# Optimization experiments

Measured on AMD Instinct MI355X. Metric: run time of the kernel, lower is better.

## Reference

```python
import jax, jax.numpy as jnp
import numpy as np

N_NODES = 100000
MAX_DEG = 128
BATCH = 16384
NUM_SAMPLES = 25


def setup_inputs() -> dict:
    key = jax.random.key(0)
    k1, k2, k3 = jax.random.split(key, 3)
    adj_weight = jax.random.uniform(k1, (N_NODES, MAX_DEG), dtype=jnp.float32)
    adj_info = jax.random.randint(k2, (N_NODES, MAX_DEG), 0, N_NODES, dtype=jnp.int32)
    ids = jax.random.randint(k3, (BATCH,), 0, N_NODES, dtype=jnp.int64)
    return {
        "adj_weight": adj_weight,
        "adj_info": adj_info,
        "ids": ids,
        "num_samples": NUM_SAMPLES,
    }


def reference(adj_weight, adj_info, ids, num_samples):
    # Gather per-node neighbor lists and weights: [B, max_deg]
    adj_lists = adj_info[ids]
    adj_weight_lists = adj_weight[ids]
    # tf.multinomial(tf.log(w), num_samples): categorical sampling with
    # replacement, probabilities proportional to weights.
    logits = jnp.log(adj_weight_lists)  # [B, max_deg]
    skey = jax.random.key(42)
    # categorical over last axis; draw num_samples per row -> [B, num_samples]
    idx = jax.random.categorical(
        skey, logits, axis=-1, shape=(num_samples, ids.shape[0])
    ).T
    # Gather sampled neighbor ids (equivalent to the flattened bias+gather trick)
    res = jnp.take_along_axis(adj_lists, idx, axis=1)  # [B, num_samples]
    return res
```

## Files before the change

kernel.cpp:

```cpp
#include <hip/hip_runtime.h>
#include <stdint.h>


#define MAXDEG 128

__device__ __forceinline__ uint32_t rotl32(uint32_t x, int r) {
  return __builtin_rotateleft32(x, r);
}

__device__ __forceinline__ uint32_t tf_bits(uint32_t i) {
  uint32_t x0, x1;
  x1 = i + 42u;
  x0 = x1;
  x1 = rotl32(x1, 13) ^ x0;
  x0 += x1; x1 = rotl32(x1, 15) ^ x0;
  x0 += x1; x1 = rotl32(x1, 26) ^ x0;
  x0 += x1; x1 = rotl32(x1,  6) ^ x0;
  x1 += 0x1BD11BF1u; x0 = x0 + x1 + 42u;
  x1 = rotl32(x1, 17) ^ x0;
  x0 += x1; x1 = rotl32(x1, 29) ^ x0;
  x0 += x1; x1 = rotl32(x1, 16) ^ x0;
  x0 += x1; x1 = rotl32(x1, 24) ^ x0;
  x1 += 2u; x0 = x0 + x1 + 0x1BD11BF0u;
  x1 = rotl32(x1, 13) ^ x0;
  x0 += x1; x1 = rotl32(x1, 15) ^ x0;
  x0 += x1; x1 = rotl32(x1, 26) ^ x0;
  x0 += x1; x1 = rotl32(x1,  6) ^ x0;
  x1 += 45u; x0 = x0 + x1;
  x1 = rotl32(x1, 17) ^ x0;
  x0 += x1; x1 = rotl32(x1, 29) ^ x0;
  x0 += x1; x1 = rotl32(x1, 16) ^ x0;
  x0 += x1; x1 = rotl32(x1, 24) ^ x0;
  x1 += 0x1BD11BF4u; x0 = x0 + x1 + 42u;
  x1 = rotl32(x1, 13) ^ x0;
  x0 += x1; x1 = rotl32(x1, 15) ^ x0;
  x0 += x1; x1 = rotl32(x1, 26) ^ x0;
  x0 += x1; x1 = rotl32(x1,  6) ^ x0;
  return (x0 + 0x1BD11BF0u) ^ (x1 + 5u);
}

__device__ __forceinline__ float uniform_from_bits(uint32_t bits) {
  uint32_t fb = (bits >> 9) | 0x3f800000u;
  float f = __uint_as_float(fb) - 1.0f;
  return fmaxf(f, 1.17549435e-38f);
}

__device__ __forceinline__ float zscore(float lwp, uint32_t bits) {
  const float l = __log2f(uniform_from_bits(bits));
  const float t = __log2f(-l);
  return __builtin_fmaf(-0.69314718056f, t, lwp);
}

template <int CTRL>
__device__ __forceinline__ float dpp_max_step(float z) {
  const int t = __builtin_amdgcn_update_dpp(0, __float_as_int(z), CTRL, 0xF, 0xF, true);
  return fmaxf(z, __int_as_float(t));
}

__device__ __forceinline__ float swz_max16(float z) {
  return fmaxf(z, __int_as_float(
      __builtin_amdgcn_ds_swizzle(__float_as_int(z), 0x401F)));
}

__device__ __attribute__((noinline)) void resolve_f64(
    float4 wv, uint32_t sbase, int l, int lane, int storeLane,
    const int* __restrict__ adj_info, long long nid,
    int* __restrict__ out, long long outIdx) {
  const uint32_t bits0 = tf_bits(sbase + 0u);
  const uint32_t bits1 = tf_bits(sbase + 1u);
  const uint32_t bits2 = tf_bits(sbase + 2u);
  const uint32_t bits3 = tf_bits(sbase + 3u);
  double bz = log((double)wv.x) - log(-log((double)uniform_from_bits(bits0)));
  int bd = 4 * l;
  const double Z1 = log((double)wv.y) - log(-log((double)uniform_from_bits(bits1)));
  if (Z1 > bz) { bz = Z1; bd = 4 * l + 1; }
  const double Z2 = log((double)wv.z) - log(-log((double)uniform_from_bits(bits2)));
  if (Z2 > bz) { bz = Z2; bd = 4 * l + 2; }
  const double Z3 = log((double)wv.w) - log(-log((double)uniform_from_bits(bits3)));
  if (Z3 > bz) { bz = Z3; bd = 4 * l + 3; }
  #pragma unroll
  for (int m = 1; m < 32; m <<= 1) {
    const double oz = __shfl_xor(bz, m);
    const int od = __shfl_xor(bd, m);
    if (oz > bz || (oz == bz && od < bd)) { bz = oz; bd = od; }
  }
  if (lane == storeLane) out[outIdx] = adj_info[nid * MAXDEG + bd];
}

__global__ __launch_bounds__(256, 8) void wns_kernel(
    const float* __restrict__ adj_weight,
    const int* __restrict__ adj_info,
    const int* __restrict__ ids,
    int* __restrict__ out,
    int batch, int nsamp) {
  const int lane = threadIdx.x & 63;
  const int l = lane & 31;
  const int wid = blockIdx.x * 4 + (threadIdx.x >> 6);
  if (2 * wid >= batch) return;
  const int b = 2 * wid + (lane >> 5);

  const long long nid = (long long)ids[b];
  const float4 wv = *(const float4*)(adj_weight + nid * MAXDEG + 4 * l);
  const float lwp0 = __logf(wv.x) + 0.36651292f;
  const float lwp1 = __logf(wv.y) + 0.36651292f;
  const float lwp2 = __logf(wv.z) + 0.36651292f;
  const float lwp3 = __logf(wv.w) + 0.36651292f;

  uint32_t sbase = (uint32_t)b * 128u + (uint32_t)(4 * l);
  const uint32_t sstep = (uint32_t)batch * 128u;

  uint32_t flagA = 0u, flagB = 0u;

  #pragma unroll 5
  for (int s = 0; s < nsamp; ++s, sbase += sstep) {
    const uint32_t bits0 = tf_bits(sbase + 0u);
    const uint32_t bits1 = tf_bits(sbase + 1u);
    const uint32_t bits2 = tf_bits(sbase + 2u);
    const uint32_t bits3 = tf_bits(sbase + 3u);

    const float z0 = zscore(lwp0, bits0);
    const float z1 = zscore(lwp1, bits1);
    const float z2 = zscore(lwp2, bits2);
    const float z3 = zscore(lwp3, bits3);

    float zmax = fmaxf(fmaxf(fmaxf(z0, z1), z2), z3);
    zmax = dpp_max_step<0x121>(zmax);
    zmax = dpp_max_step<0x122>(zmax);
    zmax = dpp_max_step<0x124>(zmax);
    zmax = dpp_max_step<0x128>(zmax);
    zmax = swz_max16(zmax);

    const float thr = zmax - 3.0e-4f;
    const unsigned long long m0 = __ballot(z0 > thr);
    const unsigned long long m1 = __ballot(z1 > thr);
    const unsigned long long m2 = __ballot(z2 > thr);
    const unsigned long long m3 = __ballot(z3 > thr);
    const uint32_t a0 = (uint32_t)m0, a1 = (uint32_t)m1,
                   a2 = (uint32_t)m2, a3 = (uint32_t)m3;
    const uint32_t c0 = (uint32_t)(m0 >> 32), c1 = (uint32_t)(m1 >> 32),
                   c2 = (uint32_t)(m2 >> 32), c3 = (uint32_t)(m3 >> 32);
    const int cntA = __popc(a0) + __popc(a1) + __popc(a2) + __popc(a3);
    const int cntB = __popc(c0) + __popc(c1) + __popc(c2) + __popc(c3);

    const int dA = a0 ? 4 * __builtin_ctz(a0)
                 : a1 ? 4 * __builtin_ctz(a1) + 1
                 : a2 ? 4 * __builtin_ctz(a2) + 2
                 : a3 ? 4 * __builtin_ctz(a3) + 3 : 0;
    const int dB = c0 ? 4 * __builtin_ctz(c0)
                 : c1 ? 4 * __builtin_ctz(c1) + 1
                 : c2 ? 4 * __builtin_ctz(c2) + 2
                 : c3 ? 4 * __builtin_ctz(c3) + 3 : 0;
    const int d = (lane < 32) ? dA : dB;
    if (l == 0) out[(long long)b * nsamp + s] = adj_info[nid * MAXDEG + d];

    flagA |= (cntA != 1) ? (1u << s) : 0u;
    flagB |= (cntB != 1) ? (1u << s) : 0u;
  }

  const uint32_t rowbase = (uint32_t)b * 128u + (uint32_t)(4 * l);
  for (uint32_t m = flagA; m; m &= m - 1u) {
    const int s = __builtin_ctz(m);
    resolve_f64(wv, rowbase + (uint32_t)s * sstep, l, lane, 0,
                adj_info, nid, out, (long long)b * nsamp + s);
  }
  for (uint32_t m = flagB; m; m &= m - 1u) {
    const int s = __builtin_ctz(m);
    resolve_f64(wv, rowbase + (uint32_t)s * sstep, l, lane, 32,
                adj_info, nid, out, (long long)b * nsamp + s);
  }
}

extern "C" void kernel_launch(void* const* d_in, const int* in_sizes, int n_in,
                              void* d_out, int out_size, void* d_ws, size_t ws_size,
                              hipStream_t stream) {
  const float* adj_weight = (const float*)d_in[0];
  const int* adj_info = (const int*)d_in[1];
  const int* ids = (const int*)d_in[2];
  int batch = in_sizes[2];
  int nsamp = out_size / batch;
  int waves = (batch + 1) / 2;
  int blocks = (waves + 3) / 4;
  wns_kernel<<<blocks, 256, 0, stream>>>(adj_weight, adj_info, ids,
                                         (int*)d_out, batch, nsamp);
}
```

Before: 148.5 us.

## Defer neighbor gathers and write all samples with one coalesced store

Each lane now keeps the chosen neighbor index for one sample in a register across the sampling loop, instead of lane 0 doing a dependent gather and a scalar store every iteration. After the loop, lanes 0..nsamp-1 of each half-wave each gather one adj_info entry and write one output element, so the 25 scattered stores per row become one contiguous store. The two half-wave fallback loops are merged into one loop over the union of flags, and resolve_f64 returns the index, which is broadcast with shuffles. Node ids and output offsets move to 32-bit arithmetic. This assumes nsamp is at most 32, and it may run the f64 resolve for a sample that only the other half-wave needed.

```diff
diff --git a/kernel.cpp b/kernel.cpp
--- a/kernel.cpp
+++ b/kernel.cpp
@@ -62,10 +62,8 @@
       __builtin_amdgcn_ds_swizzle(__float_as_int(z), 0x401F)));
 }
 
-__device__ __attribute__((noinline)) void resolve_f64(
-    float4 wv, uint32_t sbase, int l, int lane, int storeLane,
-    const int* __restrict__ adj_info, long long nid,
-    int* __restrict__ out, long long outIdx) {
+__device__ __attribute__((noinline)) int resolve_f64(
+    float4 wv, uint32_t sbase, int l) {
   const uint32_t bits0 = tf_bits(sbase + 0u);
   const uint32_t bits1 = tf_bits(sbase + 1u);
   const uint32_t bits2 = tf_bits(sbase + 2u);
@@ -84,7 +82,7 @@
     const int od = __shfl_xor(bd, m);
     if (oz > bz || (oz == bz && od < bd)) { bz = oz; bd = od; }
   }
-  if (lane == storeLane) out[outIdx] = adj_info[nid * MAXDEG + bd];
+  return bd;
 }
 
 __global__ __launch_bounds__(256, 8) void wns_kernel(
@@ -99,7 +97,7 @@
   if (2 * wid >= batch) return;
   const int b = 2 * wid + (lane >> 5);
 
-  const long long nid = (long long)ids[b];
+  const int nid = ids[b];
   const float4 wv = *(const float4*)(adj_weight + nid * MAXDEG + 4 * l);
   const float lwp0 = __logf(wv.x) + 0.36651292f;
   const float lwp1 = __logf(wv.y) + 0.36651292f;
@@ -110,6 +108,7 @@
   const uint32_t sstep = (uint32_t)batch * 128u;
 
   uint32_t flagA = 0u, flagB = 0u;
+  int dAcc = 0;
 
   #pragma unroll 5
   for (int s = 0; s < nsamp; ++s, sbase += sstep) {
@@ -150,23 +149,25 @@
                  : c1 ? 4 * __builtin_ctz(c1) + 1
                  : c2 ? 4 * __builtin_ctz(c2) + 2
                  : c3 ? 4 * __builtin_ctz(c3) + 3 : 0;
-    const int d = (lane < 32) ? dA : dB;
-    if (l == 0) out[(long long)b * nsamp + s] = adj_info[nid * MAXDEG + d];
+    dAcc = (lane == s) ? dA : dAcc;
+    dAcc = (lane == s + 32) ? dB : dAcc;
 
     flagA |= (cntA != 1) ? (1u << s) : 0u;
     flagB |= (cntB != 1) ? (1u << s) : 0u;
   }
 
   const uint32_t rowbase = (uint32_t)b * 128u + (uint32_t)(4 * l);
-  for (uint32_t m = flagA; m; m &= m - 1u) {
+  for (uint32_t m = flagA | flagB; m; m &= m - 1u) {
     const int s = __builtin_ctz(m);
-    resolve_f64(wv, rowbase + (uint32_t)s * sstep, l, lane, 0,
-                adj_info, nid, out, (long long)b * nsamp + s);
+    const int bd = resolve_f64(wv, rowbase + (uint32_t)s * sstep, l);
+    const int bdA = __shfl(bd, 0);
+    const int bdB = __shfl(bd, 32);
+    if (((flagA >> s) & 1u) && lane == s) dAcc = bdA;
+    if (((flagB >> s) & 1u) && lane == s + 32) dAcc = bdB;
   }
-  for (uint32_t m = flagB; m; m &= m - 1u) {
-    const int s = __builtin_ctz(m);
-    resolve_f64(wv, rowbase + (uint32_t)s * sstep, l, lane, 32,
-                adj_info, nid, out, (long long)b * nsamp + s);
+
+  if (l < nsamp) {
+    out[b * nsamp + l] = adj_info[nid * MAXDEG + dAcc];
   }
 }
 
```

Measured after the change: 146.2 us. Within noise of the previous version (-1.5%).
